# Kernel optimization log

Hardware: AMD Instinct MI355X
Metric: run time of the kernel (lower is better)

## Reference

```python
import jax, jax.numpy as jnp
import numpy as np

DIM = 256
HID = int(DIM * 2.66)        # 680
CH = 2 * HID                 # 1360, TVConv channels
K = 3
K2 = K * K
HP, WP = 14, 14
POSI = 4
INTER = min(64, HID // 2)    # 64
EPS = 1e-5


def conv2d(x, w, pad):
    # x: (B, Cin, H, W), w: (Cout, Cin, kh, kw)
    return jax.lax.conv_general_dilated(
        x, w, window_strides=(1, 1), padding=[(pad, pad), (pad, pad)],
        dimension_numbers=("NCHW", "OIHW", "NCHW"))


def layernorm_chw(x, g, b):
    # torch nn.LayerNorm([C, H, W]): normalize over last 3 dims, affine (C,H,W)
    mu = jnp.mean(x, axis=(1, 2, 3), keepdims=True)
    var = jnp.var(x, axis=(1, 2, 3), keepdims=True)
    return (x - mu) * jax.lax.rsqrt(var + EPS) * g + b


def weight_layers(posi_map, w0, g0, b0, w1, g1, b1, w2, g2, b2, wf):
    h = jax.nn.relu(layernorm_chw(conv2d(posi_map, w0, 1), g0, b0))
    h = jax.nn.relu(layernorm_chw(conv2d(h, w1, 1), g1, b1))
    h = jax.nn.relu(layernorm_chw(conv2d(h, w2, 1), g2, b2))
    return conv2d(h, wf, 1)  # (1, CH*K2, HP, WP)


def tvconv(x, weight):
    # x: (B, CH, HP, WP); weight: (1, CH, K2, HP, WP)
    B, C, H, W = x.shape
    xp = jnp.pad(x, ((0, 0), (0, 0), (1, 1), (1, 1)))
    # unfold ordering: channel-major, kernel positions row-major -> axis=2
    patches = jnp.stack([xp[:, :, i:i + H, j:j + W]
                         for i in range(K) for j in range(K)], axis=2)
    return jnp.sum(weight * patches, axis=2)  # (B, CH, H, W)


def frfn_forward(x, W_in, posi_map, w0, g0, b0, w1, g1, b1, w2, g2, b2, wf, W_out):
    h = jnp.einsum('oc,bchw->bohw', W_in, x)                      # project_in (1x1)
    wgt = weight_layers(posi_map, w0, g0, b0, w1, g1, b1, w2, g2, b2, wf)
    wgt = wgt.reshape(1, CH, K2, HP, WP)
    h = tvconv(h, wgt)                                            # (B, CH, H, W)
    x1, x2 = h[:, :HID], h[:, HID:]
    h = jax.nn.gelu(x1, approximate=False) * x2
    return jnp.einsum('oc,bchw->bohw', W_out, h)                  # project_out (1x1)


def setup_inputs() -> dict:
    key = jax.random.key(0)
    ks = jax.random.split(key, 16)
    s = 0.02
    out_chans = CH * K2
    return {
        "x": jax.random.normal(ks[0], (64, DIM, HP, WP), jnp.float32),
        "W_in": jax.random.normal(ks[1], (CH, DIM), jnp.float32) * s,
        "posi_map": jnp.ones((1, POSI, HP, WP), jnp.float32),
        "w0": jax.random.normal(ks[2], (INTER, POSI, K, K), jnp.float32) * s,
        "g0": jnp.ones((INTER, HP, WP), jnp.float32),
        "b0": jnp.zeros((INTER, HP, WP), jnp.float32),
        "w1": jax.random.normal(ks[3], (INTER, INTER, K, K), jnp.float32) * s,
        "g1": jnp.ones((INTER, HP, WP), jnp.float32),
        "b1": jnp.zeros((INTER, HP, WP), jnp.float32),
        "w2": jax.random.normal(ks[4], (INTER, INTER, K, K), jnp.float32) * s,
        "g2": jnp.ones((INTER, HP, WP), jnp.float32),
        "b2": jnp.zeros((INTER, HP, WP), jnp.float32),
        "wf": jax.random.normal(ks[5], (out_chans, INTER, K, K), jnp.float32) * s,
        "W_out": jax.random.normal(ks[6], (DIM, HID), jnp.float32) * s,
    }


def reference(x, W_in, posi_map, w0, g0, b0, w1, g1, b1, w2, g2, b2, wf, W_out):
    return frfn_forward(x, W_in, posi_map, w0, g0, b0, w1, g1, b1, w2, g2, b2, wf, W_out)
```

## Files before the change

kernel.cpp:

```cpp
#include <hip/hip_runtime.h>
#include <math.h>

#define DIMC   256
#define HID    680
#define CHN    1360
#define HP     14
#define WP     14
#define P      196
#define POSI   4
#define INTER  64
#define BATCH  64
#define KPAD   704
#define OUTCH  12240
#define MW     1408
#define MTOT   12672
#define KIM    576
#define MPADIN 1408
#define EPSLN  1e-5f

typedef __attribute__((ext_vector_type(8))) short short8;
typedef __attribute__((ext_vector_type(4))) short short4v;
typedef __attribute__((ext_vector_type(4))) float f32x4;

#define OFS_WBIN  0u
#define OFS_WBOUT 720896u
#define OFS_XT    1081344u
#define OFS_V0    7503872u
#define OFS_V1    7554048u
#define OFS_V2    7604224u
#define OFS_WGTT  7654656u
#define OFS_H1T   12452736u
#define OFS_HGT   46580608u
#define OFS_IMC   64242560u
#define OFS_WFB   64468352u
#define OFS_PST   79066496u

__device__ __forceinline__ unsigned short f2bf(float f) {
    union { float f; unsigned u; } v; v.f = f;
    unsigned u = v.u;
    return (unsigned short)((u + 0x7FFFu + ((u >> 16) & 1u)) >> 16);
}
__device__ __forceinline__ float bf2f(unsigned short h) {
    union { unsigned u; float f; } v; v.u = ((unsigned)h) << 16; return v.f;
}

__device__ __forceinline__ void gl2lds16(const unsigned short* g, unsigned short* l) {
    __builtin_amdgcn_global_load_lds(
        (const __attribute__((address_space(1))) unsigned int*)g,
        (__attribute__((address_space(3))) unsigned int*)l, 16, 0, 0);
}
__device__ __forceinline__ short8 fragld64(const unsigned short* S, int row, int lp) {
    int slot = ((row >> 1) + lp) & 7;
    return *(const short8*)(S + row * 64 + slot * 8);
}

__device__ __forceinline__ void block_reduce2(float& s, float& ss, float* red, int tid, int nthreads) {
    #pragma unroll
    for (int off = 32; off > 0; off >>= 1) {
        s  += __shfl_down(s, off);
        ss += __shfl_down(ss, off);
    }
    int wid = tid >> 6, nw = nthreads >> 6;
    if ((tid & 63) == 0) { red[wid*2] = s; red[wid*2+1] = ss; }
    __syncthreads();
    if (tid == 0) {
        float S = 0.f, SS = 0.f;
        for (int i = 0; i < nw; i++) { S += red[i*2]; SS += red[i*2+1]; }
        red[0] = S; red[1] = SS;
    }
    __syncthreads();
    s = red[0]; ss = red[1];
}

__device__ __forceinline__ void sum_pstat(const float* __restrict__ pstat, int base,
                                          float& s, float& ss) {
    s = 0.f; ss = 0.f;
    #pragma unroll
    for (int i = 0; i < 49; i++) {
        s  += pstat[base + 2*i];
        ss += pstat[base + 2*i + 1];
    }
}

#define NWIN  (MPADIN*DIMC)
#define NWOUT (DIMC*KPAD)
#define XT0   49
#define WF0   561
#define C0    2343
#define IMZ0  2475
#define PRE_BLKS 2489

__global__ __launch_bounds__(256) void k_pre(const float* __restrict__ Win,
                                             const float* __restrict__ Wout,
                                             const float* __restrict__ x,
                                             const float* __restrict__ wf,
                                             const float* __restrict__ posi,
                                             const float* __restrict__ w0,
                                             unsigned short* __restrict__ Wbin,
                                             unsigned short* __restrict__ Wbout,
                                             unsigned short* __restrict__ Xt,
                                             unsigned short* __restrict__ wfb,
                                             unsigned short* __restrict__ imc,
                                             float* __restrict__ v0,
                                             float* __restrict__ pstat) {
    __shared__ __align__(16) float smem[6304];
    int bid = blockIdx.x, tid = threadIdx.x;
    if (bid < XT0) {
        float (*ppad)[16][16] = (float(*)[16][16])smem;
        float* red = smem + 1024;
        for (int i = tid; i < POSI * 256; i += 256) {
            int cc = i >> 8, r = i & 255, ly = r >> 4, lx = r & 15;
            float v = 0.f;
            if (ly >= 1 && ly <= HP && lx >= 1 && lx <= WP) v = posi[cc*P + (ly-1)*WP + (lx-1)];
            ppad[cc][ly][lx] = v;
        }
        __syncthreads();
        int gid = bid * 256 + tid;
        int c = gid / P, p = gid - c*P, y = p / WP, x2 = p - (p/WP)*WP;
        float v = 0.f;
        #pragma unroll
        for (int ci = 0; ci < POSI; ci++) {
            const float* wr = w0 + (c*POSI + ci)*9;
            v += wr[0]*ppad[ci][y  ][x2] + wr[1]*ppad[ci][y  ][x2+1] + wr[2]*ppad[ci][y  ][x2+2]
               + wr[3]*ppad[ci][y+1][x2] + wr[4]*ppad[ci][y+1][x2+1] + wr[5]*ppad[ci][y+1][x2+2]
               + wr[6]*ppad[ci][y+2][x2] + wr[7]*ppad[ci][y+2][x2+1] + wr[8]*ppad[ci][y+2][x2+2];
        }
        v0[gid] = v;
        float s = v, ss = v * v;
        block_reduce2(s, ss, red, tid, 256);
        if (tid == 0) { pstat[2*bid] = s; pstat[2*bid + 1] = ss; }
    } else if (bid < WF0) {
        int b2 = bid - XT0;
        int b = b2 >> 3, c0 = (b2 & 7) * 32;
        float (*xs)[197] = (float(*)[197])smem;
        for (int i = tid; i < 32 * P; i += 256) {
            int ci = i / P, pp = i - ci * P;
            xs[ci][pp] = x[((size_t)b * DIMC + c0 + ci) * P + pp];
        }
        __syncthreads();
        for (int j = tid; j < P * 32; j += 256) {
            int ci = j & 31, pp = j >> 5;
            Xt[((size_t)b * P + pp) * DIMC + c0 + ci] = f2bf(xs[ci][pp]);
        }
    } else if (bid < C0) {
        int base = (bid - WF0) * 1024;
        #pragma unroll
        for (int k2 = 0; k2 < 4; k2++) {
            int t = base + k2 * 256 + tid;
            int j = t * 4;
            int rowi = j / KIM, q = j - rowi * KIM;
            int kk = rowi / MW, ch = rowi - kk * MW;
            short4v sv = (short4v)0;
            if (ch < CHN) {
                float4 v = *(const float4*)(wf + ((size_t)(ch * 9 + kk)) * KIM + q);
                sv[0] = (short)f2bf(v.x); sv[1] = (short)f2bf(v.y);
                sv[2] = (short)f2bf(v.z); sv[3] = (short)f2bf(v.w);
            }
            *(short4v*)(wfb + j) = sv;
        }
    } else if (bid < IMZ0) {
        int base = (bid - C0) * 1024;
        #pragma unroll
        for (int k2 = 0; k2 < 4; k2++) {
            int t = base + k2 * 256 + tid;
            int i0 = t * 4;
            if (i0 < NWIN) {
                short4v sv = (short4v)0;
                if (i0 < CHN * DIMC) {
                    float4 v = *(const float4*)(Win + i0);
                    sv[0] = (short)f2bf(v.x); sv[1] = (short)f2bf(v.y);
                    sv[2] = (short)f2bf(v.z); sv[3] = (short)f2bf(v.w);
                }
                *(short4v*)(Wbin + i0) = sv;
            } else {
                int j0 = i0 - NWIN;
                int o = j0 / KPAD, k = j0 - o * KPAD;
                short4v sv = (short4v)0;
                if (k < HID) {
                    float4 v = *(const float4*)(Wout + o * HID + k);
                    sv[0] = (short)f2bf(v.x); sv[1] = (short)f2bf(v.y);
                    sv[2] = (short)f2bf(v.z); sv[3] = (short)f2bf(v.w);
                }
                *(short4v*)(Wbout + j0) = sv;
            }
        }
    } else {
        int base = (bid - IMZ0) * 1024;
        #pragma unroll
        for (int k2 = 0; k2 < 4; k2++) {
            int cc = base + k2 * 256 + tid;
            if (cc < (P * KIM) / 8) *(short8*)(imc + cc * 8) = (short8)0;
        }
    }
}


__device__ __forceinline__ void dev_convln(char* sm, int bid, int tid,
                                           const float* __restrict__ v_in,
                                           const float* __restrict__ g,
                                           const float* __restrict__ b,
                                           const float* __restrict__ w,
                                           float* __restrict__ v_out,
                                           float* __restrict__ pstat,
                                           int psi, int pso) {
    float* asf = (float*)sm;
    float* wlf = asf + INTER * 256;
    float* red = wlf + 3 * INTER * 12;
    const float inv = 1.f / (float)(INTER * P);
    float s0, ss0;
    sum_pstat(pstat, psi, s0, ss0);
    float mu = s0 * inv;
    float var = ss0 * inv - mu * mu;
    float rstd = rsqrtf(var + EPSLN);

    int gid0 = bid * 256;
    int cA = gid0 / P;
    for (int i = tid; i < 3 * INTER * 9; i += 256) {
        int cc = i / (INTER * 9), rest = i - cc * (INTER * 9);
        int ci = rest / 9, kk = rest - ci * 9;
        int crow = cA + cc; if (crow >= INTER) crow = INTER - 1;
        wlf[cc * (INTER * 12) + ci * 12 + kk] = w[(crow * INTER + ci) * 9 + kk];
    }
    for (int i = tid; i < INTER * 64; i += 256)
        *(f32x4*)(asf + i * 4) = (f32x4)0.f;
    __syncthreads();
    #pragma unroll
    for (int it = 0; it < 13; it++) {
        int q4 = it * 256 + tid;
        if (q4 < (INTER * P) / 4) {
            float4 vv = *(const float4*)(v_in + q4 * 4);
            float4 gg = *(const float4*)(g + q4 * 4);
            float4 bb = *(const float4*)(b + q4 * 4);
            float va[4] = {vv.x, vv.y, vv.z, vv.w};
            float ga[4] = {gg.x, gg.y, gg.z, gg.w};
            float ba[4] = {bb.x, bb.y, bb.z, bb.w};
            #pragma unroll
            for (int e = 0; e < 4; e++) {
                int idx = q4 * 4 + e;
                int ci = idx / P, p = idx - ci * P;
                int yy = p / WP, xx = p - yy * WP;
                float a = (va[e] - mu) * rstd * ga[e] + ba[e];
                asf[ci * 256 + (yy + 1) * 16 + (xx + 1)] = a > 0.f ? a : 0.f;
            }
        }
    }
    __syncthreads();
    int gid = gid0 + tid;
    int c = gid / P, p = gid - c * P, y = p / WP, x = p - (p / WP) * WP;
    const float* wr0 = wlf + (c - cA) * (INTER * 12);
    float v = 0.f;
    for (int ci = 0; ci < INTER; ci++) {
        const float* wi = wr0 + ci * 12;
        const float* a0 = asf + ci * 256 + y * 16 + x;
        v += wi[0]*a0[0]  + wi[1]*a0[1]  + wi[2]*a0[2]
           + wi[3]*a0[16] + wi[4]*a0[17] + wi[5]*a0[18]
           + wi[6]*a0[32] + wi[7]*a0[33] + wi[8]*a0[34];
    }
    v_out[gid] = v;
    float s = v, ss = v * v;
    block_reduce2(s, ss, red, tid, 256);
    if (tid == 0) { pstat[pso + 2*bid] = s; pstat[pso + 2*bid + 1] = ss; }
}

__device__ __forceinline__ void dev_lnsc(int bid, int tid,
                                         const float* __restrict__ v_in,
                                         const float* __restrict__ g,
                                         const float* __restrict__ b,
                                         const float* __restrict__ pstat,
                                         unsigned short* __restrict__ imc) {
    const float inv = 1.f / (float)(INTER * P);
    int gid = bid * 256 + tid;
    float s0, ss0;
    sum_pstat(pstat, 196, s0, ss0);
    float mu = s0 * inv;
    float var = ss0 * inv - mu * mu;
    float rstd = rsqrtf(var + EPSLN);
    float a = (v_in[gid] - mu) * rstd * g[gid] + b[gid];
    a = a > 0.f ? a : 0.f;
    unsigned short bv = f2bf(a);
    int ci = gid / P, p = gid - ci * P, y = p / WP, x = p - (p / WP) * WP;
    #pragma unroll
    for (int k = 0; k < 9; k++) {
        int yp = y - (k / 3 - 1), xp = x - (k % 3 - 1);
        if (yp >= 0 && yp < HP && xp >= 0 && xp < WP)
            imc[(yp * WP + xp) * KIM + ci * 9 + k] = bv;
    }
}

__device__ __forceinline__ void dev_gemm_in(char* sm, int mb, int nb, int tid,
                                            const unsigned short* __restrict__ A,
                                            const unsigned short* __restrict__ B,
                                            unsigned short* __restrict__ C) {
    unsigned short* As = (unsigned short*)sm;
    unsigned short* Bs = As + 128 * 64;
    int w = tid >> 6, lane = tid & 63, quad = lane >> 4, c16 = lane & 15;
    int m0 = mb * 128, n0 = nb * 128;
    int wm = (w & 1) * 64, wn = (w >> 1) * 64;
    f32x4 acc[4][4];
    #pragma unroll
    for (int i = 0; i < 4; i++)
        #pragma unroll
        for (int j = 0; j < 4; j++) acc[i][j] = (f32x4)0.f;

    for (int kc = 0; kc < 4; ++kc) {
        int k0 = kc * 64;
        if (kc) __syncthreads();
        #pragma unroll
        for (int i = tid; i < 1024; i += 256) {
            int r = i >> 3, s = i & 7, q = (s - (r >> 1)) & 7;
            gl2lds16(A + (size_t)(m0 + r) * DIMC + k0 + q * 8, As + (i & ~63) * 8);
        }
        #pragma unroll
        for (int i = tid; i < 1024; i += 256) {
            int r = i >> 3, s = i & 7, q = (s - (r >> 1)) & 7;
            gl2lds16(B + (size_t)(n0 + r) * DIMC + k0 + q * 8, Bs + (i & ~63) * 8);
        }
        __syncthreads();
        #pragma unroll
        for (int ks = 0; ks < 2; ++ks) {
            short8 af[4], bfr[4];
            #pragma unroll
            for (int i = 0; i < 4; i++) af[i] = fragld64(As, wm + i * 16 + c16, ks * 4 + quad);
            #pragma unroll
            for (int j = 0; j < 4; j++) bfr[j] = fragld64(Bs, wn + j * 16 + c16, ks * 4 + quad);
            #pragma unroll
            for (int i = 0; i < 4; i++)
                #pragma unroll
                for (int j = 0; j < 4; j++)
                    acc[i][j] = __builtin_amdgcn_mfma_f32_16x16x32_bf16(af[i], bfr[j], acc[i][j], 0, 0, 0);
        }
    }
    #pragma unroll
    for (int j = 0; j < 4; j++) {
        int n = n0 + wn + j * 16 + c16;
        unsigned short* dst = C + (size_t)n * CHN;
        #pragma unroll
        for (int i = 0; i < 4; i++) {
            int m = m0 + wm + i * 16 + quad * 4;
            if (m < CHN) {
                short4v sv;
                sv[0] = (short)f2bf(acc[i][j][0]);
                sv[1] = (short)f2bf(acc[i][j][1]);
                sv[2] = (short)f2bf(acc[i][j][2]);
                sv[3] = (short)f2bf(acc[i][j][3]);
                *(short4v*)(dst + m) = sv;
            }
        }
    }
}

__device__ __forceinline__ void dev_gemm_wf(char* sm, int bid, int tid,
                                            const unsigned short* __restrict__ wfb,
                                            const unsigned short* __restrict__ imc,
                                            unsigned short* __restrict__ wgtT) {
    unsigned short* buf = (unsigned short*)sm;
    unsigned short* As = buf;
    unsigned short* Bs = buf + 64 * 64;
    unsigned short* ot = buf;
    int w = tid >> 6, lane = tid & 63, quad = lane >> 4, c16 = lane & 15;
    int m0 = bid * 64;
    int kk = m0 / MW, ch0 = m0 - kk * MW;
    for (int i = tid; i < 96; i += 256)
        *(short8*)(Bs + 196 * 64 + i * 8) = (short8)0;
    f32x4 acc[13];
    #pragma unroll
    for (int f = 0; f < 13; f++) acc[f] = (f32x4)0.f;

    for (int kc = 0; kc < 9; ++kc) {
        int k0 = kc * 64;
        if (kc) __syncthreads();
        #pragma unroll
        for (int i = tid; i < 512; i += 256) {
            int r = i >> 3, s = i & 7, q = (s - (r >> 1)) & 7;
            gl2lds16(wfb + ((size_t)(kk * MW + ch0 + r)) * KIM + k0 + q * 8, As + (i & ~63) * 8);
        }
        for (int i = tid; i < 1568; i += 256) {
            int r = i >> 3, s = i & 7, q = (s - (r >> 1)) & 7;
            gl2lds16(imc + (size_t)r * KIM + k0 + q * 8, Bs + (i & ~63) * 8);
        }
        __syncthreads();
        #pragma unroll
        for (int ks = 0; ks < 2; ++ks) {
            short8 af = fragld64(As, w * 16 + c16, ks * 4 + quad);
            #pragma unroll
            for (int f = 0; f < 13; f++) {
                short8 bf = fragld64(Bs, f * 16 + c16, ks * 4 + quad);
                acc[f] = __builtin_amdgcn_mfma_f32_16x16x32_bf16(af, bf, acc[f], 0, 0, 0);
            }
        }
    }
    __syncthreads();
    #pragma unroll
    for (int f = 0; f < 13; f++) {
        int p = f * 16 + c16;
        if (p < P) {
            short4v sv;
            sv[0] = (short)f2bf(acc[f][0]);
            sv[1] = (short)f2bf(acc[f][1]);
            sv[2] = (short)f2bf(acc[f][2]);
            sv[3] = (short)f2bf(acc[f][3]);
            *(short4v*)(ot + p * 72 + w * 16 + quad * 4) = sv;
        }
    }
    __syncthreads();
    int nvalid = CHN - ch0; if (nvalid > 64) nvalid = 64;
    for (int p = tid; p < P; p += 256) {
        const short8* src = (const short8*)(ot + p * 72);
        unsigned short* dst = wgtT + ((size_t)p * 9 + kk) * CHN + ch0;
        #pragma unroll
        for (int j = 0; j < 8; j++)
            if (j * 8 < nvalid) *(short8*)(dst + j * 8) = src[j];
    }
}

#define SLICE 210
#define CONVLN_LDS ((INTER*256 + 3*INTER*12 + 16) * 4)
#define GEMMWF_LDS ((64*64 + 208*64) * 2)

extern __shared__ char dynsm[];

__global__ __launch_bounds__(256) void k_mA(const float* v0, const float* g0,
                                            const float* b0, const float* w1,
                                            float* v1, float* pstat,
                                            const unsigned short* Wbin,
                                            const unsigned short* Xt,
                                            unsigned short* h1t) {
    int bid = blockIdx.x, tid = threadIdx.x;
    if (bid < 49) dev_convln(dynsm, bid, tid, v0, g0, b0, w1, v1, pstat, 0, 98);
    else { int fid = bid - 49; dev_gemm_in(dynsm, fid % 11, fid / 11, tid, Wbin, Xt, h1t); }
}
__global__ __launch_bounds__(256) void k_mB(const float* v1, const float* g1,
                                            const float* b1, const float* w2,
                                            float* v2, float* pstat,
                                            const unsigned short* Wbin,
                                            const unsigned short* Xt,
                                            unsigned short* h1t) {
    int bid = blockIdx.x, tid = threadIdx.x;
    if (bid < 49) dev_convln(dynsm, bid, tid, v1, g1, b1, w2, v2, pstat, 98, 196);
    else { int fid = SLICE + bid - 49; dev_gemm_in(dynsm, fid % 11, fid / 11, tid, Wbin, Xt, h1t); }
}
__global__ __launch_bounds__(256) void k_mC(const float* v2, const float* g2,
                                            const float* b2, const float* pstat,
                                            unsigned short* imc,
                                            const unsigned short* Wbin,
                                            const unsigned short* Xt,
                                            unsigned short* h1t) {
    int bid = blockIdx.x, tid = threadIdx.x;
    if (bid < 49) dev_lnsc(bid, tid, v2, g2, b2, pstat, imc);
    else { int fid = 2 * SLICE + bid - 49; dev_gemm_in(dynsm, fid % 11, fid / 11, tid, Wbin, Xt, h1t); }
}
__global__ __launch_bounds__(256) void k_mD(const unsigned short* wfb,
                                            const unsigned short* imc,
                                            unsigned short* wgtT,
                                            const unsigned short* Wbin,
                                            const unsigned short* Xt,
                                            unsigned short* h1t) {
    int bid = blockIdx.x, tid = threadIdx.x;
    if (bid < 198) dev_gemm_wf(dynsm, bid, tid, wfb, imc, wgtT);
    else { int fid = 3 * SLICE + bid - 198; dev_gemm_in(dynsm, fid % 11, fid / 11, tid, Wbin, Xt, h1t); }
}

__global__ __launch_bounds__(256) void k_tvg(const unsigned short* __restrict__ h1t,
                                             const unsigned short* __restrict__ wgtT,
                                             unsigned short* __restrict__ hgt) {
    __shared__ __align__(16) unsigned short wl[9 * CHN];
    int id = blockIdx.x;
    int xcd = id & 7, q = id >> 3;
    int p = xcd * 25 + (q % 25);
    int bg = q / 25;
    if (p >= P) return;
    int b0 = bg * 8, tid = threadIdx.x;
    const unsigned short* wrow = wgtT + (size_t)p * 9 * CHN;
    for (int i = tid * 8; i < 9 * CHN; i += 256 * 8)
        *(short8*)(wl + i) = *(const short8*)(wrow + i);
    int y = p / WP, x = p - (p / WP) * WP;
    int pn[9]; bool pv[9];
    #pragma unroll
    for (int k = 0; k < 9; k++) {
        int yy = y + k / 3 - 1, xx = x + (k % 3) - 1;
        pv[k] = (yy >= 0 && yy < HP && xx >= 0 && xx < WP);
        pn[k] = pv[k] ? yy * WP + xx : 0;
    }
    __syncthreads();
    for (int j = tid; j < 8 * 85; j += 256) {
        int bl = j / 85, c = (j - bl * 85) * 8;
        int b = b0 + bl;
        const unsigned short* hb = h1t + (size_t)b * P * CHN;
        float s1[8], s2[8];
        #pragma unroll
        for (int e = 0; e < 8; e++) { s1[e] = 0.f; s2[e] = 0.f; }
        #pragma unroll
        for (int k = 0; k < 9; k++) {
            if (!pv[k]) continue;
            const unsigned short* hr = hb + (size_t)pn[k] * CHN + c;
            short8 h1v = *(const short8*)hr;
            short8 h2v = *(const short8*)(hr + HID);
            short8 w1v = *(const short8*)(wl + k * CHN + c);
            short8 w2v = *(const short8*)(wl + k * CHN + HID + c);
            #pragma unroll
            for (int e = 0; e < 8; e++) {
                s1[e] += bf2f((unsigned short)w1v[e]) * bf2f((unsigned short)h1v[e]);
                s2[e] += bf2f((unsigned short)w2v[e]) * bf2f((unsigned short)h2v[e]);
            }
        }
        short8 o;
        #pragma unroll
        for (int e = 0; e < 8; e++) {
            float gl = 0.5f * s1[e] * (1.f + erff(s1[e] * 0.70710678118654752f));
            o[e] = (short)f2bf(gl * s2[e]);
        }
        *(short8*)(hgt + ((size_t)b * P + p) * KPAD + c) = o;
    }
    if (tid < 24) {
        int bl = tid / 3, z = (tid - bl * 3) * 8;
        *(short8*)(hgt + ((size_t)(b0 + bl) * P + p) * KPAD + HID + z) = (short8)0;
    }
}

__global__ __launch_bounds__(256) void k_gemm_out(const unsigned short* __restrict__ A,
                                                  const unsigned short* __restrict__ B,
                                                  float* __restrict__ out) {
    __shared__ __align__(16) unsigned short As[64 * 64];
    __shared__ __align__(16) unsigned short Bs[128 * 64];
    int tid = threadIdx.x;
    int w = tid >> 6, lane = tid & 63, quad = lane >> 4, c16 = lane & 15;
    int m0 = blockIdx.x * 64, n0 = blockIdx.y * 128;
    int wm = (w & 1) * 32, wn = (w >> 1) * 64;
    f32x4 acc[2][4];
    #pragma unroll
    for (int i = 0; i < 2; i++)
        #pragma unroll
        for (int j = 0; j < 4; j++) acc[i][j] = (f32x4)0.f;

    for (int kc = 0; kc < 11; ++kc) {
        int k0 = kc * 64;
        if (kc) __syncthreads();
        #pragma unroll
        for (int i = tid; i < 512; i += 256) {
            int r = i >> 3, s = i & 7, q = (s - (r >> 1)) & 7;
            gl2lds16(A + (size_t)(m0 + r) * KPAD + k0 + q * 8, As + (i & ~63) * 8);
        }
        #pragma unroll
        for (int i = tid; i < 1024; i += 256) {
            int r = i >> 3, s = i & 7, q = (s - (r >> 1)) & 7;
            gl2lds16(B + (size_t)(n0 + r) * KPAD + k0 + q * 8, Bs + (i & ~63) * 8);
        }
        __syncthreads();
        #pragma unroll
        for (int ks = 0; ks < 2; ++ks) {
            short8 af[2], bfr[4];
            #pragma unroll
            for (int i = 0; i < 2; i++) af[i] = fragld64(As, wm + i * 16 + c16, ks * 4 + quad);
            #pragma unroll
            for (int j = 0; j < 4; j++) bfr[j] = fragld64(Bs, wn + j * 16 + c16, ks * 4 + quad);
            #pragma unroll
            for (int i = 0; i < 2; i++)
                #pragma unroll
                for (int j = 0; j < 4; j++)
                    acc[i][j] = __builtin_amdgcn_mfma_f32_16x16x32_bf16(af[i], bfr[j], acc[i][j], 0, 0, 0);
        }
    }
    #pragma unroll
    for (int j = 0; j < 4; j++) {
        int n = n0 + wn + j * 16 + c16;
        int b = n / P, pp = n - b * P;
        #pragma unroll
        for (int i = 0; i < 2; i++) {
            int m = m0 + wm + i * 16 + quad * 4;
            #pragma unroll
            for (int r = 0; r < 4; r++)
                out[((size_t)b * DIMC + m + r) * P + pp] = acc[i][j][r];
        }
    }
}

extern "C" void kernel_launch(void* const* d_in, const int* in_sizes, int n_in,
                              void* d_out, int out_size, void* d_ws, size_t ws_size,
                              hipStream_t stream) {
    (void)in_sizes; (void)n_in; (void)out_size; (void)ws_size;
    const float* x     = (const float*)d_in[0];
    const float* W_in  = (const float*)d_in[1];
    const float* posi  = (const float*)d_in[2];
    const float* w0    = (const float*)d_in[3];
    const float* g0    = (const float*)d_in[4];
    const float* b0    = (const float*)d_in[5];
    const float* w1    = (const float*)d_in[6];
    const float* g1    = (const float*)d_in[7];
    const float* b1    = (const float*)d_in[8];
    const float* w2    = (const float*)d_in[9];
    const float* g2    = (const float*)d_in[10];
    const float* b2    = (const float*)d_in[11];
    const float* wf    = (const float*)d_in[12];
    const float* W_out = (const float*)d_in[13];
    float* out = (float*)d_out;
    char* ws = (char*)d_ws;

    unsigned short* Wbin  = (unsigned short*)(ws + OFS_WBIN);
    unsigned short* Wbout = (unsigned short*)(ws + OFS_WBOUT);
    unsigned short* Xt    = (unsigned short*)(ws + OFS_XT);
    float*          v0    = (float*)(ws + OFS_V0);
    float*          v1    = (float*)(ws + OFS_V1);
    float*          v2    = (float*)(ws + OFS_V2);
    float*          pstat = (float*)(ws + OFS_PST);
    unsigned short* wgtT  = (unsigned short*)(ws + OFS_WGTT);
    unsigned short* h1t   = (unsigned short*)(ws + OFS_H1T);
    unsigned short* hgt   = (unsigned short*)(ws + OFS_HGT);
    unsigned short* imc   = (unsigned short*)(ws + OFS_IMC);
    unsigned short* wfb   = (unsigned short*)(ws + OFS_WFB);

    k_pre<<<PRE_BLKS, 256, 0, stream>>>(
        W_in, W_out, x, wf, posi, w0, Wbin, Wbout, Xt, wfb, imc, v0, pstat);
    k_mA<<<49 + SLICE, 256, CONVLN_LDS, stream>>>(v0, g0, b0, w1, v1, pstat, Wbin, Xt, h1t);
    k_mB<<<49 + SLICE, 256, CONVLN_LDS, stream>>>(v1, g1, b1, w2, v2, pstat, Wbin, Xt, h1t);
    k_mC<<<49 + SLICE, 256, CONVLN_LDS, stream>>>(v2, g2, b2, pstat, imc, Wbin, Xt, h1t);
    k_mD<<<198 + 448, 256, GEMMWF_LDS, stream>>>(wfb, imc, wgtT, Wbin, Xt, h1t);
    k_tvg     <<<1600, 256, 0, stream>>>(h1t, wgtT, hgt);
    k_gemm_out<<<dim3(DIMC/64, (BATCH*P)/128), 256, 0, stream>>>(Wbout, hgt, out);
}
```

Baseline: 217.9 us.

## Enlarge GEMM tiles, vectorize input transpose, and double per-block batch in tvconv

The input projection GEMM moves from 128x128 to 128x256 tiles, giving each wave 4x8 accumulators, and the GEMM slices spread across the fused kernels are halved to match. The output GEMM grows to 128x128 tiles, and the tvconv kernel now handles 16 batches per block with half as many blocks. The x transpose now uses float4 loads and 16-byte bf16 stores. The aim is more data reuse and fewer blocks, at the cost of higher register pressure, fewer blocks to fill the device, and a larger LDS footprint that k_mD now sizes with GIN_LDS.

```diff
diff --git a/kernel.cpp b/kernel.cpp
--- a/kernel.cpp
+++ b/kernel.cpp
@@ -132,15 +132,20 @@
     } else if (bid < WF0) {
         int b2 = bid - XT0;
         int b = b2 >> 3, c0 = (b2 & 7) * 32;
-        float (*xs)[197] = (float(*)[197])smem;
-        for (int i = tid; i < 32 * P; i += 256) {
-            int ci = i / P, pp = i - ci * P;
-            xs[ci][pp] = x[((size_t)b * DIMC + c0 + ci) * P + pp];
+        float* xs = smem;
+        for (int i = tid; i < 32 * 49; i += 256) {
+            int ci = i / 49, p4 = (i - ci * 49) * 4;
+            float4 v = *(const float4*)(x + ((size_t)b * DIMC + c0 + ci) * P + p4);
+            float* d = xs + ci * 197 + p4;
+            d[0] = v.x; d[1] = v.y; d[2] = v.z; d[3] = v.w;
         }
         __syncthreads();
-        for (int j = tid; j < P * 32; j += 256) {
-            int ci = j & 31, pp = j >> 5;
-            Xt[((size_t)b * P + pp) * DIMC + c0 + ci] = f2bf(xs[ci][pp]);
+        for (int j = tid; j < P * 4; j += 256) {
+            int pp = j >> 2, c8 = (j & 3) * 8;
+            short8 o;
+            #pragma unroll
+            for (int e = 0; e < 8; e++) o[e] = (short)f2bf(xs[(c8 + e) * 197 + pp]);
+            *(short8*)(Xt + ((size_t)b * P + pp) * DIMC + c0 + c8) = o;
         }
     } else if (bid < C0) {
         int base = (bid - WF0) * 1024;
@@ -287,6 +292,9 @@
     }
 }
 
+#define GIN_MT 11
+#define GIN_NT 49
+#define GIN_BLKS (GIN_MT * GIN_NT)
 __device__ __forceinline__ void dev_gemm_in(char* sm, int mb, int nb, int tid,
                                             const unsigned short* __restrict__ A,
                                             const unsigned short* __restrict__ B,
@@ -294,13 +302,13 @@
     unsigned short* As = (unsigned short*)sm;
     unsigned short* Bs = As + 128 * 64;
     int w = tid >> 6, lane = tid & 63, quad = lane >> 4, c16 = lane & 15;
-    int m0 = mb * 128, n0 = nb * 128;
-    int wm = (w & 1) * 64, wn = (w >> 1) * 64;
-    f32x4 acc[4][4];
+    int m0 = mb * 128, n0 = nb * 256;
+    int wm = (w & 1) * 64, wn = (w >> 1) * 128;
+    f32x4 acc[4][8];
     #pragma unroll
     for (int i = 0; i < 4; i++)
         #pragma unroll
-        for (int j = 0; j < 4; j++) acc[i][j] = (f32x4)0.f;
+        for (int j = 0; j < 8; j++) acc[i][j] = (f32x4)0.f;
 
     for (int kc = 0; kc < 4; ++kc) {
         int k0 = kc * 64;
@@ -311,27 +319,27 @@
             gl2lds16(A + (size_t)(m0 + r) * DIMC + k0 + q * 8, As + (i & ~63) * 8);
         }
         #pragma unroll
-        for (int i = tid; i < 1024; i += 256) {
+        for (int i = tid; i < 2048; i += 256) {
             int r = i >> 3, s = i & 7, q = (s - (r >> 1)) & 7;
             gl2lds16(B + (size_t)(n0 + r) * DIMC + k0 + q * 8, Bs + (i & ~63) * 8);
         }
         __syncthreads();
         #pragma unroll
         for (int ks = 0; ks < 2; ++ks) {
-            short8 af[4], bfr[4];
+            short8 af[4];
             #pragma unroll
             for (int i = 0; i < 4; i++) af[i] = fragld64(As, wm + i * 16 + c16, ks * 4 + quad);
             #pragma unroll
-            for (int j = 0; j < 4; j++) bfr[j] = fragld64(Bs, wn + j * 16 + c16, ks * 4 + quad);
-            #pragma unroll
-            for (int i = 0; i < 4; i++)
+            for (int j = 0; j < 8; j++) {
+                short8 bf = fragld64(Bs, wn + j * 16 + c16, ks * 4 + quad);
                 #pragma unroll
-                for (int j = 0; j < 4; j++)
-                    acc[i][j] = __builtin_amdgcn_mfma_f32_16x16x32_bf16(af[i], bfr[j], acc[i][j], 0, 0, 0);
-        }
-    }
-    #pragma unroll
-    for (int j = 0; j < 4; j++) {
+                for (int i = 0; i < 4; i++)
+                    acc[i][j] = __builtin_amdgcn_mfma_f32_16x16x32_bf16(af[i], bf, acc[i][j], 0, 0, 0);
+            }
+        }
+    }
+    #pragma unroll
+    for (int j = 0; j < 8; j++) {
         int n = n0 + wn + j * 16 + c16;
         unsigned short* dst = C + (size_t)n * CHN;
         #pragma unroll
@@ -413,9 +421,9 @@
     }
 }
 
-#define SLICE 210
+#define SLICE 105
 #define CONVLN_LDS ((INTER*256 + 3*INTER*12 + 16) * 4)
-#define GEMMWF_LDS ((64*64 + 208*64) * 2)
+#define GIN_LDS    ((128*64 + 256*64) * 2)
 
 extern __shared__ char dynsm[];
 
@@ -427,7 +435,7 @@
                                             unsigned short* h1t) {
     int bid = blockIdx.x, tid = threadIdx.x;
     if (bid < 49) dev_convln(dynsm, bid, tid, v0, g0, b0, w1, v1, pstat, 0, 98);
-    else { int fid = bid - 49; dev_gemm_in(dynsm, fid % 11, fid / 11, tid, Wbin, Xt, h1t); }
+    else { int fid = bid - 49; dev_gemm_in(dynsm, fid % GIN_MT, fid / GIN_MT, tid, Wbin, Xt, h1t); }
 }
 __global__ __launch_bounds__(256) void k_mB(const float* v1, const float* g1,
                                             const float* b1, const float* w2,
@@ -437,7 +445,7 @@
                                             unsigned short* h1t) {
     int bid = blockIdx.x, tid = threadIdx.x;
     if (bid < 49) dev_convln(dynsm, bid, tid, v1, g1, b1, w2, v2, pstat, 98, 196);
-    else { int fid = SLICE + bid - 49; dev_gemm_in(dynsm, fid % 11, fid / 11, tid, Wbin, Xt, h1t); }
+    else { int fid = SLICE + bid - 49; dev_gemm_in(dynsm, fid % GIN_MT, fid / GIN_MT, tid, Wbin, Xt, h1t); }
 }
 __global__ __launch_bounds__(256) void k_mC(const float* v2, const float* g2,
                                             const float* b2, const float* pstat,
@@ -447,7 +455,7 @@
                                             unsigned short* h1t) {
     int bid = blockIdx.x, tid = threadIdx.x;
     if (bid < 49) dev_lnsc(bid, tid, v2, g2, b2, pstat, imc);
-    else { int fid = 2 * SLICE + bid - 49; dev_gemm_in(dynsm, fid % 11, fid / 11, tid, Wbin, Xt, h1t); }
+    else { int fid = 2 * SLICE + bid - 49; dev_gemm_in(dynsm, fid % GIN_MT, fid / GIN_MT, tid, Wbin, Xt, h1t); }
 }
 __global__ __launch_bounds__(256) void k_mD(const unsigned short* wfb,
                                             const unsigned short* imc,
@@ -457,7 +465,7 @@
                                             unsigned short* h1t) {
     int bid = blockIdx.x, tid = threadIdx.x;
     if (bid < 198) dev_gemm_wf(dynsm, bid, tid, wfb, imc, wgtT);
-    else { int fid = 3 * SLICE + bid - 198; dev_gemm_in(dynsm, fid % 11, fid / 11, tid, Wbin, Xt, h1t); }
+    else { int fid = 3 * SLICE + bid - 198; dev_gemm_in(dynsm, fid % GIN_MT, fid / GIN_MT, tid, Wbin, Xt, h1t); }
 }
 
 __global__ __launch_bounds__(256) void k_tvg(const unsigned short* __restrict__ h1t,
@@ -469,7 +477,7 @@
     int p = xcd * 25 + (q % 25);
     int bg = q / 25;
     if (p >= P) return;
-    int b0 = bg * 8, tid = threadIdx.x;
+    int b0 = bg * 16, tid = threadIdx.x;
     const unsigned short* wrow = wgtT + (size_t)p * 9 * CHN;
     for (int i = tid * 8; i < 9 * CHN; i += 256 * 8)
         *(short8*)(wl + i) = *(const short8*)(wrow + i);
@@ -482,7 +490,7 @@
         pn[k] = pv[k] ? yy * WP + xx : 0;
     }
     __syncthreads();
-    for (int j = tid; j < 8 * 85; j += 256) {
+    for (int j = tid; j < 16 * 85; j += 256) {
         int bl = j / 85, c = (j - bl * 85) * 8;
         int b = b0 + bl;
         const unsigned short* hb = h1t + (size_t)b * P * CHN;
@@ -511,7 +519,7 @@
         }
         *(short8*)(hgt + ((size_t)b * P + p) * KPAD + c) = o;
     }
-    if (tid < 24) {
+    if (tid < 48) {
         int bl = tid / 3, z = (tid - bl * 3) * 8;
         *(short8*)(hgt + ((size_t)(b0 + bl) * P + p) * KPAD + HID + z) = (short8)0;
     }
@@ -520,15 +528,15 @@
 __global__ __launch_bounds__(256) void k_gemm_out(const unsigned short* __restrict__ A,
                                                   const unsigned short* __restrict__ B,
                                                   float* __restrict__ out) {
-    __shared__ __align__(16) unsigned short As[64 * 64];
+    __shared__ __align__(16) unsigned short As[128 * 64];
     __shared__ __align__(16) unsigned short Bs[128 * 64];
     int tid = threadIdx.x;
     int w = tid >> 6, lane = tid & 63, quad = lane >> 4, c16 = lane & 15;
-    int m0 = blockIdx.x * 64, n0 = blockIdx.y * 128;
-    int wm = (w & 1) * 32, wn = (w >> 1) * 64;
-    f32x4 acc[2][4];
-    #pragma unroll
-    for (int i = 0; i < 2; i++)
+    int m0 = blockIdx.x * 128, n0 = blockIdx.y * 128;
+    int wm = (w & 1) * 64, wn = (w >> 1) * 64;
+    f32x4 acc[4][4];
+    #pragma unroll
+    for (int i = 0; i < 4; i++)
         #pragma unroll
         for (int j = 0; j < 4; j++) acc[i][j] = (f32x4)0.f;
 
@@ -536,7 +544,7 @@
         int k0 = kc * 64;
         if (kc) __syncthreads();
         #pragma unroll
-        for (int i = tid; i < 512; i += 256) {
+        for (int i = tid; i < 1024; i += 256) {
             int r = i >> 3, s = i & 7, q = (s - (r >> 1)) & 7;
             gl2lds16(A + (size_t)(m0 + r) * KPAD + k0 + q * 8, As + (i & ~63) * 8);
         }
@@ -548,13 +556,13 @@
         __syncthreads();
         #pragma unroll
         for (int ks = 0; ks < 2; ++ks) {
-            short8 af[2], bfr[4];
-            #pragma unroll
-            for (int i = 0; i < 2; i++) af[i] = fragld64(As, wm + i * 16 + c16, ks * 4 + quad);
+            short8 af[4], bfr[4];
+            #pragma unroll
+            for (int i = 0; i < 4; i++) af[i] = fragld64(As, wm + i * 16 + c16, ks * 4 + quad);
             #pragma unroll
             for (int j = 0; j < 4; j++) bfr[j] = fragld64(Bs, wn + j * 16 + c16, ks * 4 + quad);
             #pragma unroll
-            for (int i = 0; i < 2; i++)
+            for (int i = 0; i < 4; i++)
                 #pragma unroll
                 for (int j = 0; j < 4; j++)
                     acc[i][j] = __builtin_amdgcn_mfma_f32_16x16x32_bf16(af[i], bfr[j], acc[i][j], 0, 0, 0);
@@ -565,7 +573,7 @@
         int n = n0 + wn + j * 16 + c16;
         int b = n / P, pp = n - b * P;
         #pragma unroll
-        for (int i = 0; i < 2; i++) {
+        for (int i = 0; i < 4; i++) {
             int m = m0 + wm + i * 16 + quad * 4;
             #pragma unroll
             for (int r = 0; r < 4; r++)
@@ -613,7 +621,7 @@
     k_mA<<<49 + SLICE, 256, CONVLN_LDS, stream>>>(v0, g0, b0, w1, v1, pstat, Wbin, Xt, h1t);
     k_mB<<<49 + SLICE, 256, CONVLN_LDS, stream>>>(v1, g1, b1, w2, v2, pstat, Wbin, Xt, h1t);
     k_mC<<<49 + SLICE, 256, CONVLN_LDS, stream>>>(v2, g2, b2, pstat, imc, Wbin, Xt, h1t);
-    k_mD<<<198 + 448, 256, GEMMWF_LDS, stream>>>(wfb, imc, wgtT, Wbin, Xt, h1t);
-    k_tvg     <<<1600, 256, 0, stream>>>(h1t, wgtT, hgt);
-    k_gemm_out<<<dim3(DIMC/64, (BATCH*P)/128), 256, 0, stream>>>(Wbout, hgt, out);
-}
+    k_mD<<<198 + (GIN_BLKS - 3 * SLICE), 256, GIN_LDS, stream>>>(wfb, imc, wgtT, Wbin, Xt, h1t);
+    k_tvg     <<<800, 256, 0, stream>>>(h1t, wgtT, hgt);
+    k_gemm_out<<<dim3(DIMC/128, (BATCH*P)/128), 256, 0, stream>>>(Wbout, hgt, out);
+}
```

New measurement: 235.1 us. 1.08x slower.
